# Optimization experiments

Hardware: AMD Instinct MI355X
Metric: run time of the kernel (lower is better)

The kernel has to match this reference:

```python
import jax, jax.numpy as jnp
import numpy as np

B, N, T, D = 8, 64, 50, 4      # batch, atoms, timesteps, features per node
K, H = 2, 64                   # edge types, hidden (msg_hid = msg_out = n_hid)
START = 1                      # skip_first_edge_type=True
E = N * (N - 1)


def setup_inputs() -> dict:
    key = jax.random.key(0)
    ks = jax.random.split(key, 10)
    # fully-connected relation graph: all ordered pairs i != j
    recv_idx, send_idx = np.where(~np.eye(N, dtype=bool))
    eye = np.eye(N, dtype=np.float32)
    rel_rec = jnp.asarray(eye[recv_idx])    # [E, N] one-hot receivers
    rel_send = jnp.asarray(eye[send_idx])   # [E, N] one-hot senders
    s = 0.1
    return {
        "inputs": jax.random.normal(ks[0], (B, N, T, D), jnp.float32),
        "rel_type": jax.random.uniform(ks[1], (B, 1, E, K), jnp.float32),
        "rel_rec": rel_rec,
        "rel_send": rel_send,
        "fc1_w": jax.random.normal(ks[2], (K, H, 2 * D), jnp.float32) * s,
        "fc1_b": jnp.zeros((K, H), jnp.float32),
        "fc2_w": jax.random.normal(ks[3], (K, H, H), jnp.float32) * s,
        "fc2_b": jnp.zeros((K, H), jnp.float32),
        "out1_w": jax.random.normal(ks[4], (H, D + H), jnp.float32) * s,
        "out1_b": jnp.zeros((H,), jnp.float32),
        "out2_w": jax.random.normal(ks[5], (H, H), jnp.float32) * s,
        "out2_b": jnp.zeros((H,), jnp.float32),
        "out3_w": jax.random.normal(ks[6], (D, H), jnp.float32) * s,
        "out3_b": jnp.zeros((D,), jnp.float32),
        "pred_steps": 1,
    }


def reference(inputs, rel_type, rel_rec, rel_send,
              fc1_w, fc1_b, fc2_w, fc2_b,
              out1_w, out1_b, out2_w, out2_b, out3_w, out3_b,
              pred_steps):
    assert pred_steps == 1
    x_in = jnp.swapaxes(inputs, 1, 2)  # [B, T, N, D]
    t = x_in.shape[1]
    # rel_type [B,1,E,K] -> expand over time
    rt = jnp.broadcast_to(rel_type, (rel_type.shape[0], t) + rel_type.shape[2:])

    # node2edge: gather receivers/senders via one-hot matmuls
    recv = jnp.einsum('en,btnd->bted', rel_rec, x_in)
    send = jnp.einsum('en,btnd->bted', rel_send, x_in)
    pre_msg = jnp.concatenate([recv, send], axis=-1)  # [B,T,E,2D]

    # per-edge-type MLP, masked by inferred edge prob, accumulated
    all_msgs = jnp.zeros(pre_msg.shape[:3] + (H,), pre_msg.dtype)
    for i in range(START, K):
        h = jax.nn.relu(jnp.einsum('bted,hd->bteh', pre_msg, fc1_w[i]) + fc1_b[i])
        m = jax.nn.relu(jnp.einsum('bteh,oh->bteo', h, fc2_w[i]) + fc2_b[i])
        all_msgs = all_msgs + m * rt[..., i:i + 1]

    # edge2node: scatter-accumulate to receivers via one-hot transpose matmul
    agg = jnp.einsum('en,bteh->btnh', rel_rec, all_msgs)  # [B,T,N,H]

    aug = jnp.concatenate([x_in, agg], axis=-1)           # [B,T,N,D+H]
    h = jax.nn.relu(jnp.einsum('btni,oi->btno', aug, out1_w) + out1_b)
    h = jax.nn.relu(jnp.einsum('btni,oi->btno', h, out2_w) + out2_b)
    delta = jnp.einsum('btni,oi->btno', h, out3_w) + out3_b
    x_tp1 = x_in + delta                                  # predict_delta=True

    pred_all = x_tp1[:, :t - 1]                           # [B,T-1,N,D]
    return jnp.swapaxes(pred_all, 1, 2)                   # [B,N,T-1,D]
```

## Files before the change

### kernel.cpp

```cpp
#include <hip/hip_runtime.h>


#define NB 8
#define NN 64
#define NT 50
#define NTO 49
#define ND 4
#define NE 4032

typedef _Float16 f16x8 __attribute__((ext_vector_type(8)));
typedef _Float16 f16x2 __attribute__((ext_vector_type(2)));
typedef float f32x4 __attribute__((ext_vector_type(4)));

union Frag8 { unsigned u[4]; f16x8 f; f16x2 h[4]; };

#define MFMA16(A, B, C) __builtin_amdgcn_mfma_f32_16x16x32_f16((A), (B), (C), 0, 0, 0)

#define WS_VG   0u
#define WS_PG   3211264u
#define WS_RTG  6422528u
#define WS_W2F  6553600u
#define WS_B1F  6561792u
#define WS_B2F  6569984u
#define WS_B3F  6578176u

__global__ __launch_bounds__(64) void nri_prep_kernel(
    const float* __restrict__ inputs,
    const float* __restrict__ rel_type,
    const float* __restrict__ fc1_w,
    const float* __restrict__ fc1_b,
    const float* __restrict__ fc2_w,
    const float* __restrict__ out1_w,
    const float* __restrict__ out2_w,
    const float* __restrict__ out3_w,
    char* __restrict__ ws)
{
  _Float16* const Vg  = (_Float16*)(ws + WS_VG);
  _Float16* const Pg  = (_Float16*)(ws + WS_PG);
  float*    const rtg = (float*)   (ws + WS_RTG);
  _Float16* const W2f = (_Float16*)(ws + WS_W2F);
  _Float16* const B1f = (_Float16*)(ws + WS_B1F);
  _Float16* const B2f = (_Float16*)(ws + WS_B2F);
  _Float16* const B3f = (_Float16*)(ws + WS_B3F);

  const int bid = blockIdx.x;
  const int g   = bid & 7;
  const int t   = (bid >> 3) % NTO;
  const int b   = bid / (8 * NTO);
  const int k   = threadIdx.x;
  const int bt64 = (b * NTO + t) * 64;

  const float4 w1r = *(const float4*)(fc1_w + 512 + k * 8);
  const float4 w1s = *(const float4*)(fc1_w + 516 + k * 8);
  const float  b1k = fc1_b[64 + k];

  if (g < 4) {
#pragma unroll
    for (int ii = 0; ii < 16; ++ii) {
      const int s = g * 16 + ii;
      const float4 x = *(const float4*)(inputs + ((b * NN + s) * NT + t) * ND);
      Vg[(bt64 + s) * 64 + k] =
          (_Float16)(w1s.x*x.x + w1s.y*x.y + w1s.z*x.z + w1s.w*x.w);
    }
  } else {
#pragma unroll
    for (int ii = 0; ii < 16; ++ii) {
      const int n = (g - 4) * 16 + ii;
      const float4 x = *(const float4*)(inputs + ((b * NN + n) * NT + t) * ND);
      Pg[(bt64 + n) * 64 + k] =
          (_Float16)(b1k + w1r.x*x.x + w1r.y*x.y + w1r.z*x.z + w1r.w*x.w);
    }
  }

  if (t == 0) {
#pragma unroll
    for (int ii = 0; ii < 8; ++ii) {
      const int n = g * 8 + ii;
      const int s = k;
      const float v = (s == n) ? 0.f
                    : rel_type[(b * NE + n * 63 + (s < n ? s : s - 1)) * 2 + 1];
      rtg[(b * 64 + n) * 64 + s] = v;
    }
  }
  if (b == 0 && t == 0) {
    if (g == 0) {
      for (int o = 0; o < 64; ++o)
        W2f[o * 64 + k] = (_Float16)fc2_w[4096 + o * 64 + k];
    } else if (g == 1) {
      for (int o = 0; o < 64; ++o)
        B1f[o * 64 + k] = (_Float16)out1_w[o * 68 + 4 + k];
    } else if (g == 2) {
      for (int o = 0; o < 64; ++o)
        B2f[o * 64 + k] = (_Float16)out2_w[o * 64 + k];
    } else if (g == 3) {
      for (int d = 0; d < 4; ++d)
        B3f[d * 64 + k] = (_Float16)out3_w[d * 64 + k];
    }
  }
}

__global__ __launch_bounds__(256) void nri_main_kernel(
    const float* __restrict__ inputs,
    const float* __restrict__ fc2_b,
    const float* __restrict__ out1_w,
    const float* __restrict__ out1_b,
    const float* __restrict__ out2_b,
    const float* __restrict__ out3_b,
    const char* __restrict__ ws,
    float* __restrict__ out)
{
  const _Float16* const Vg  = (const _Float16*)(ws + WS_VG);
  const _Float16* const Pg  = (const _Float16*)(ws + WS_PG);
  const float*    const rtg = (const float*)   (ws + WS_RTG);
  const _Float16* const W2f = (const _Float16*)(ws + WS_W2F);
  const _Float16* const B1f = (const _Float16*)(ws + WS_B1F);
  const _Float16* const B2f = (const _Float16*)(ws + WS_B2F);
  const _Float16* const B3f = (const _Float16*)(ws + WS_B3F);

  __shared__ _Float16 AggH[16 * 68];
  __shared__ _Float16 H1L[16 * 68];
  __shared__ _Float16 H2L[16 * 68];
  __shared__ float4   Xl[16];

  const int bid    = blockIdx.x;
  const int tile   = bid & 3;
  const int t      = (bid >> 2) % NTO;
  const int b      = bid / (4 * NTO);
  const int n_base = tile * 16;
  const int tid  = threadIdx.x;
  const int lane = tid & 63;
  const int w    = tid >> 6;
  const int q    = lane >> 4;
  const int r    = lane & 15;
  const int bt64 = (b * NTO + t) * 64;

  if (tid < 16)
    Xl[tid] = *(const float4*)(inputs + ((b * NN + n_base + tid) * NT + t) * ND);

  Frag8 va[4][2];
#pragma unroll
  for (int st = 0; st < 4; ++st) {
    const _Float16* vp = Vg + (bt64 + st * 16 + r) * 64 + q * 8;
    va[st][0].f = *(const f16x8*)vp;
    va[st][1].f = *(const f16x8*)(vp + 32);
  }
  Frag8 bfr[4][2];
  float b2l[4];
#pragma unroll
  for (int nt = 0; nt < 4; ++nt) {
    b2l[nt] = fc2_b[64 + nt * 16 + r];
    const _Float16* p = W2f + (nt * 16 + r) * 64 + q * 8;
    bfr[nt][0].f = *(const f16x8*)p;
    bfr[nt][1].f = *(const f16x8*)(p + 32);
  }
  const int o = w * 16 + r;
  Frag8 B1[2], B2[2];
  {
    const _Float16* p1 = B1f + o * 64 + q * 8;
    B1[0].f = *(const f16x8*)p1;
    B1[1].f = *(const f16x8*)(p1 + 32);
    const _Float16* p2 = B2f + o * 64 + q * 8;
    B2[0].f = *(const f16x8*)p2;
    B2[1].f = *(const f16x8*)(p2 + 32);
  }
  const float4 w1x = *(const float4*)(out1_w + o * 68);
  const float b1o = out1_b[o];
  const float b2o = out2_b[o];

#pragma unroll 1
  for (int np = 0; np < 4; ++np) {
    const int ni = w * 4 + np;
    const int n  = n_base + ni;
    Frag8 pa0, pa1;
    {
      const _Float16* pp = Pg + (bt64 + n) * 64 + q * 8;
      pa0.f = *(const f16x8*)pp;
      pa1.f = *(const f16x8*)(pp + 32);
    }
    float4 rtv[4];
#pragma unroll
    for (int st = 0; st < 4; ++st)
      rtv[st] = *(const float4*)(rtg + (b * 64 + n) * 64 + st * 16 + q * 4);

    float m0 = 0.f, m1 = 0.f, m2 = 0.f, m3 = 0.f;
#pragma unroll
    for (int st = 0; st < 4; ++st) {
      Frag8 a0, a1;
      const f16x2 z = {(_Float16)0.f, (_Float16)0.f};
#pragma unroll
      for (int j = 0; j < 4; ++j) {
        a0.h[j] = __builtin_elementwise_max((f16x2)(pa0.h[j] + va[st][0].h[j]), z);
        a1.h[j] = __builtin_elementwise_max((f16x2)(pa1.h[j] + va[st][1].h[j]), z);
      }

      f32x4 d0 = {b2l[0], b2l[0], b2l[0], b2l[0]};
      f32x4 d1 = {b2l[1], b2l[1], b2l[1], b2l[1]};
      f32x4 d2 = {b2l[2], b2l[2], b2l[2], b2l[2]};
      f32x4 d3 = {b2l[3], b2l[3], b2l[3], b2l[3]};
      d0 = MFMA16(a0.f, bfr[0][0].f, d0); d0 = MFMA16(a1.f, bfr[0][1].f, d0);
      d1 = MFMA16(a0.f, bfr[1][0].f, d1); d1 = MFMA16(a1.f, bfr[1][1].f, d1);
      d2 = MFMA16(a0.f, bfr[2][0].f, d2); d2 = MFMA16(a1.f, bfr[2][1].f, d2);
      d3 = MFMA16(a0.f, bfr[3][0].f, d3); d3 = MFMA16(a1.f, bfr[3][1].f, d3);

      const float rtf[4] = {rtv[st].x, rtv[st].y, rtv[st].z, rtv[st].w};
#pragma unroll
      for (int e = 0; e < 4; ++e) {
        m0 = fmaf(rtf[e], fmaxf(d0[e], 0.f), m0);
        m1 = fmaf(rtf[e], fmaxf(d1[e], 0.f), m1);
        m2 = fmaf(rtf[e], fmaxf(d2[e], 0.f), m2);
        m3 = fmaf(rtf[e], fmaxf(d3[e], 0.f), m3);
      }
    }
    m0 += __shfl_xor(m0, 16); m0 += __shfl_xor(m0, 32);
    m1 += __shfl_xor(m1, 16); m1 += __shfl_xor(m1, 32);
    m2 += __shfl_xor(m2, 16); m2 += __shfl_xor(m2, 32);
    m3 += __shfl_xor(m3, 16); m3 += __shfl_xor(m3, 32);
    const float aval = (q == 0) ? m0 : (q == 1) ? m1 : (q == 2) ? m2 : m3;
    AggH[ni * 68 + lane] = (_Float16)aval;
  }
  __syncthreads();

  {
    Frag8 A0, A1;
    A0.f = *(const f16x8*)(AggH + r * 68 + q * 8);
    A1.f = *(const f16x8*)(AggH + r * 68 + 32 + q * 8);
    f32x4 d = {b1o, b1o, b1o, b1o};
    d = MFMA16(A0.f, B1[0].f, d);
    d = MFMA16(A1.f, B1[1].f, d);
#pragma unroll
    for (int reg = 0; reg < 4; ++reg) {
      const int n = q * 4 + reg;
      const float4 x = Xl[n];
      const float hv = d[reg] + x.x*w1x.x + x.y*w1x.y + x.z*w1x.z + x.w*w1x.w;
      H1L[n * 68 + o] = (_Float16)fmaxf(hv, 0.f);
    }
  }
  __syncthreads();

  {
    Frag8 A0, A1;
    A0.f = *(const f16x8*)(H1L + r * 68 + q * 8);
    A1.f = *(const f16x8*)(H1L + r * 68 + 32 + q * 8);
    f32x4 d = {b2o, b2o, b2o, b2o};
    d = MFMA16(A0.f, B2[0].f, d);
    d = MFMA16(A1.f, B2[1].f, d);
#pragma unroll
    for (int reg = 0; reg < 4; ++reg) {
      const int n = q * 4 + reg;
      H2L[n * 68 + o] = (_Float16)fmaxf(d[reg], 0.f);
    }
  }
  __syncthreads();

  if (w == 0) {
    Frag8 B3[2];
    {
      const _Float16* p3 = B3f + (r & 3) * 64 + q * 8;
      B3[0].f = *(const f16x8*)p3;
      B3[1].f = *(const f16x8*)(p3 + 32);
    }
    Frag8 A0, A1;
    A0.f = *(const f16x8*)(H2L + r * 68 + q * 8);
    A1.f = *(const f16x8*)(H2L + r * 68 + 32 + q * 8);
    const float b3o = out3_b[r & 3];
    f32x4 d = {b3o, b3o, b3o, b3o};
    d = MFMA16(A0.f, B3[0].f, d);
    d = MFMA16(A1.f, B3[1].f, d);
    if (r < 4) {
      const float* xf = (const float*)Xl;
#pragma unroll
      for (int reg = 0; reg < 4; ++reg) {
        const int n = q * 4 + reg;
        out[((b * NN + n_base + n) * NTO + t) * ND + r] = xf[n * 4 + r] + d[reg];
      }
    }
  }
}

extern "C" void kernel_launch(void* const* d_in, const int* in_sizes, int n_in,
                              void* d_out, int out_size, void* d_ws, size_t ws_size,
                              hipStream_t stream) {
  const float* inputs   = (const float*)d_in[0];
  const float* rel_type = (const float*)d_in[1];
  const float* fc1_w  = (const float*)d_in[4];
  const float* fc1_b  = (const float*)d_in[5];
  const float* fc2_w  = (const float*)d_in[6];
  const float* fc2_b  = (const float*)d_in[7];
  const float* out1_w = (const float*)d_in[8];
  const float* out1_b = (const float*)d_in[9];
  const float* out2_w = (const float*)d_in[10];
  const float* out2_b = (const float*)d_in[11];
  const float* out3_w = (const float*)d_in[12];
  const float* out3_b = (const float*)d_in[13];
  float* out = (float*)d_out;
  char* ws = (char*)d_ws;

  nri_prep_kernel<<<NB * NTO * 8, 64, 0, stream>>>(
      inputs, rel_type, fc1_w, fc1_b, fc2_w, out1_w, out2_w, out3_w, ws);
  nri_main_kernel<<<NB * NTO * 4, 256, 0, stream>>>(
      inputs, fc2_b, out1_w, out1_b, out2_b, out3_b, ws, out);
}
```

Before: 131.4 us.

## Split main kernel into single-wave blocks of four nodes each

```diff
diff --git a/kernel.cpp b/kernel.cpp
--- a/kernel.cpp
+++ b/kernel.cpp
@@ -99,7 +99,7 @@
   }
 }
 
-__global__ __launch_bounds__(256) void nri_main_kernel(
+__global__ __launch_bounds__(64, 4) void nri_main_kernel(
     const float* __restrict__ inputs,
     const float* __restrict__ fc2_b,
     const float* __restrict__ out1_w,
@@ -117,25 +117,17 @@
   const _Float16* const B2f = (const _Float16*)(ws + WS_B2F);
   const _Float16* const B3f = (const _Float16*)(ws + WS_B3F);
 
-  __shared__ _Float16 AggH[16 * 68];
-  __shared__ _Float16 H1L[16 * 68];
-  __shared__ _Float16 H2L[16 * 68];
-  __shared__ float4   Xl[16];
+  __shared__ _Float16 TB[16 * 72];
 
   const int bid    = blockIdx.x;
-  const int tile   = bid & 3;
-  const int t      = (bid >> 2) % NTO;
-  const int b      = bid / (4 * NTO);
-  const int n_base = tile * 16;
-  const int tid  = threadIdx.x;
-  const int lane = tid & 63;
-  const int w    = tid >> 6;
+  const int tile   = bid & 15;
+  const int t      = (bid >> 4) % NTO;
+  const int b      = bid / (16 * NTO);
+  const int n_base = tile * 4;
+  const int lane = threadIdx.x;
   const int q    = lane >> 4;
   const int r    = lane & 15;
   const int bt64 = (b * NTO + t) * 64;
-
-  if (tid < 16)
-    Xl[tid] = *(const float4*)(inputs + ((b * NN + n_base + tid) * NT + t) * ND);
 
   Frag8 va[4][2];
 #pragma unroll
@@ -153,24 +145,10 @@
     bfr[nt][0].f = *(const f16x8*)p;
     bfr[nt][1].f = *(const f16x8*)(p + 32);
   }
-  const int o = w * 16 + r;
-  Frag8 B1[2], B2[2];
-  {
-    const _Float16* p1 = B1f + o * 64 + q * 8;
-    B1[0].f = *(const f16x8*)p1;
-    B1[1].f = *(const f16x8*)(p1 + 32);
-    const _Float16* p2 = B2f + o * 64 + q * 8;
-    B2[0].f = *(const f16x8*)p2;
-    B2[1].f = *(const f16x8*)(p2 + 32);
-  }
-  const float4 w1x = *(const float4*)(out1_w + o * 68);
-  const float b1o = out1_b[o];
-  const float b2o = out2_b[o];
 
 #pragma unroll 1
   for (int np = 0; np < 4; ++np) {
-    const int ni = w * 4 + np;
-    const int n  = n_base + ni;
+    const int n = n_base + np;
     Frag8 pa0, pa1;
     {
       const _Float16* pp = Pg + (bt64 + n) * 64 + q * 8;
@@ -192,7 +170,6 @@
         a0.h[j] = __builtin_elementwise_max((f16x2)(pa0.h[j] + va[st][0].h[j]), z);
         a1.h[j] = __builtin_elementwise_max((f16x2)(pa1.h[j] + va[st][1].h[j]), z);
       }
-
       f32x4 d0 = {b2l[0], b2l[0], b2l[0], b2l[0]};
       f32x4 d1 = {b2l[1], b2l[1], b2l[1], b2l[1]};
       f32x4 d2 = {b2l[2], b2l[2], b2l[2], b2l[2]};
@@ -216,62 +193,85 @@
     m2 += __shfl_xor(m2, 16); m2 += __shfl_xor(m2, 32);
     m3 += __shfl_xor(m3, 16); m3 += __shfl_xor(m3, 32);
     const float aval = (q == 0) ? m0 : (q == 1) ? m1 : (q == 2) ? m2 : m3;
-    AggH[ni * 68 + lane] = (_Float16)aval;
+    TB[np * 72 + lane] = (_Float16)aval;
   }
   __syncthreads();
+
+  float4 xr[4];
+#pragma unroll
+  for (int i = 0; i < 4; ++i)
+    xr[i] = *(const float4*)(inputs + ((b * NN + n_base + i) * NT + t) * ND);
 
   {
     Frag8 A0, A1;
-    A0.f = *(const f16x8*)(AggH + r * 68 + q * 8);
-    A1.f = *(const f16x8*)(AggH + r * 68 + 32 + q * 8);
-    f32x4 d = {b1o, b1o, b1o, b1o};
-    d = MFMA16(A0.f, B1[0].f, d);
-    d = MFMA16(A1.f, B1[1].f, d);
-#pragma unroll
-    for (int reg = 0; reg < 4; ++reg) {
-      const int n = q * 4 + reg;
-      const float4 x = Xl[n];
-      const float hv = d[reg] + x.x*w1x.x + x.y*w1x.y + x.z*w1x.z + x.w*w1x.w;
-      H1L[n * 68 + o] = (_Float16)fmaxf(hv, 0.f);
+    A0.f = *(const f16x8*)(TB + r * 72 + q * 8);
+    A1.f = *(const f16x8*)(TB + r * 72 + 32 + q * 8);
+#pragma unroll
+    for (int ct = 0; ct < 4; ++ct) {
+      const int o = ct * 16 + r;
+      Frag8 B0, B1;
+      const _Float16* pb = B1f + o * 64 + q * 8;
+      B0.f = *(const f16x8*)pb;
+      B1.f = *(const f16x8*)(pb + 32);
+      const float  b1o = out1_b[o];
+      const float4 w1x = *(const float4*)(out1_w + o * 68);
+      f32x4 d = {b1o, b1o, b1o, b1o};
+      d = MFMA16(A0.f, B0.f, d);
+      d = MFMA16(A1.f, B1.f, d);
+      if (q == 0) {
+#pragma unroll
+        for (int reg = 0; reg < 4; ++reg) {
+          const float4 x = xr[reg];
+          const float hv = d[reg] + x.x*w1x.x + x.y*w1x.y + x.z*w1x.z + x.w*w1x.w;
+          TB[reg * 72 + o] = (_Float16)fmaxf(hv, 0.f);
+        }
+      }
     }
   }
   __syncthreads();
 
   {
     Frag8 A0, A1;
-    A0.f = *(const f16x8*)(H1L + r * 68 + q * 8);
-    A1.f = *(const f16x8*)(H1L + r * 68 + 32 + q * 8);
-    f32x4 d = {b2o, b2o, b2o, b2o};
-    d = MFMA16(A0.f, B2[0].f, d);
-    d = MFMA16(A1.f, B2[1].f, d);
-#pragma unroll
-    for (int reg = 0; reg < 4; ++reg) {
-      const int n = q * 4 + reg;
-      H2L[n * 68 + o] = (_Float16)fmaxf(d[reg], 0.f);
+    A0.f = *(const f16x8*)(TB + r * 72 + q * 8);
+    A1.f = *(const f16x8*)(TB + r * 72 + 32 + q * 8);
+    __syncthreads();
+#pragma unroll
+    for (int ct = 0; ct < 4; ++ct) {
+      const int o = ct * 16 + r;
+      Frag8 B0, B1;
+      const _Float16* pb = B2f + o * 64 + q * 8;
+      B0.f = *(const f16x8*)pb;
+      B1.f = *(const f16x8*)(pb + 32);
+      const float b2o = out2_b[o];
+      f32x4 d = {b2o, b2o, b2o, b2o};
+      d = MFMA16(A0.f, B0.f, d);
+      d = MFMA16(A1.f, B1.f, d);
+      if (q == 0) {
+#pragma unroll
+        for (int reg = 0; reg < 4; ++reg)
+          TB[reg * 72 + o] = (_Float16)fmaxf(d[reg], 0.f);
+      }
     }
   }
   __syncthreads();
 
-  if (w == 0) {
-    Frag8 B3[2];
-    {
-      const _Float16* p3 = B3f + (r & 3) * 64 + q * 8;
-      B3[0].f = *(const f16x8*)p3;
-      B3[1].f = *(const f16x8*)(p3 + 32);
-    }
+  {
     Frag8 A0, A1;
-    A0.f = *(const f16x8*)(H2L + r * 68 + q * 8);
-    A1.f = *(const f16x8*)(H2L + r * 68 + 32 + q * 8);
+    A0.f = *(const f16x8*)(TB + r * 72 + q * 8);
+    A1.f = *(const f16x8*)(TB + r * 72 + 32 + q * 8);
+    Frag8 B0, B1;
+    const _Float16* pb = B3f + (r & 3) * 64 + q * 8;
+    B0.f = *(const f16x8*)pb;
+    B1.f = *(const f16x8*)(pb + 32);
     const float b3o = out3_b[r & 3];
     f32x4 d = {b3o, b3o, b3o, b3o};
-    d = MFMA16(A0.f, B3[0].f, d);
-    d = MFMA16(A1.f, B3[1].f, d);
-    if (r < 4) {
-      const float* xf = (const float*)Xl;
+    d = MFMA16(A0.f, B0.f, d);
+    d = MFMA16(A1.f, B1.f, d);
+    if (q == 0 && r < 4) {
 #pragma unroll
       for (int reg = 0; reg < 4; ++reg) {
-        const int n = q * 4 + reg;
-        out[((b * NN + n_base + n) * NTO + t) * ND + r] = xf[n * 4 + r] + d[reg];
+        const float xs = inputs[((b * NN + n_base + reg) * NT + t) * ND + r];
+        out[((b * NN + n_base + reg) * NTO + t) * ND + r] = xs + d[reg];
       }
     }
   }
@@ -297,6 +297,6 @@
 
   nri_prep_kernel<<<NB * NTO * 8, 64, 0, stream>>>(
       inputs, rel_type, fc1_w, fc1_b, fc2_w, out1_w, out2_w, out3_w, ws);
-  nri_main_kernel<<<NB * NTO * 4, 256, 0, stream>>>(
+  nri_main_kernel<<<NB * NTO * 16, 64, 0, stream>>>(
       inputs, fc2_b, out1_w, out1_b, out2_b, out3_b, ws, out);
 }
```

After: 162.5 us. 23.6% more time.
